# Performance work log

Hardware: AMD Instinct MI355X
Metric: run time of the kernel (lower is better)

## Reference

```python
import jax, jax.numpy as jnp
import numpy as np

N_WIRES = 12
DEPTH = 4
IN_DIM = 256
BATCH = 4096


def _apply_rx(state, theta, wire, n):
    """Apply RX(theta) = [[cos(t/2), -i sin(t/2)], [-i sin(t/2), cos(t/2)]] on `wire`.
    state: (batch, 2^n) complex. theta: scalar or (batch,) float."""
    half = theta * 0.5
    c = jnp.reshape(jnp.cos(half), (-1, 1, 1))  # broadcasts for scalar or per-batch
    s = jnp.reshape(jnp.sin(half), (-1, 1, 1))
    L, R = 2 ** wire, 2 ** (n - wire - 1)
    st = state.reshape(-1, L, 2, R)
    a0, a1 = st[:, :, 0], st[:, :, 1]
    b0 = c * a0 - 1j * s * a1
    b1 = -1j * s * a0 + c * a1
    return jnp.stack([b0, b1], axis=2).reshape(state.shape)


def _apply_cnot_adj(state, ctrl, n):
    """CNOT with control=ctrl, target=ctrl+1 (adjacent wires)."""
    L, R = 2 ** ctrl, 2 ** (n - ctrl - 2)
    st = state.reshape(-1, L, 2, 2, R)
    c0 = st[:, :, 0]
    c1 = st[:, :, 1, ::-1]  # flip target bit when control=1
    return jnp.stack([c0, c1], axis=2).reshape(state.shape)


def _pauli_z_signs(n):
    idx = np.arange(2 ** n)
    # wire 0 is the most-significant bit (torchquantum convention)
    bits = (idx[:, None] >> (n - 1 - np.arange(n))[None, :]) & 1
    return (1.0 - 2.0 * bits).astype(np.float32)  # (2^n, n)


def setup_inputs() -> dict:
    key = jax.random.key(0)
    k1, k2, k3 = jax.random.split(key, 3)
    x = jax.random.normal(k1, (BATCH, IN_DIM), dtype=jnp.float32)
    W = jax.random.normal(k2, (N_WIRES, IN_DIM), dtype=jnp.float32)
    params = jax.random.normal(k3, (DEPTH, N_WIRES, 1), dtype=jnp.float32)
    return {"x": x, "W": W, "params": params}


def reference(x, W, params):
    n = W.shape[0]
    depth = params.shape[0]
    batch = x.shape[0]
    angles = x @ W.T  # (batch, n) -- nn.Linear without bias
    state = jnp.zeros((batch, 2 ** n), dtype=jnp.complex64).at[:, 0].set(1.0)
    # data-encoding RX layer (per-batch angles)
    for w in range(n):
        state = _apply_rx(state, angles[:, w], w, n)
    # variational layers: RX(params) then CNOT ladder
    for d in range(depth):
        for w in range(n):
            state = _apply_rx(state, params[d, w, 0], w, n)
        for w in range(n - 1):
            state = _apply_cnot_adj(state, w, n)
    probs = jnp.real(state * jnp.conj(state))  # (batch, 2^n)
    signs = jnp.asarray(_pauli_z_signs(n))     # (2^n, n)
    return probs @ signs  # <Z_w> per wire, (batch, n)
```

## Files before the change

### kernel.cpp

```cpp
#include <hip/hip_runtime.h>
#include <math.h>

#define N_WIRES 12
#define DEPTH   4
#define IN_DIM  256
#define NK      4096
#define ROWS_PER_BLOCK 16
#define XSTRIDE 272


struct MaskTable {
    unsigned m[DEPTH * N_WIRES];
    unsigned S[N_WIRES];
};

__global__ __launch_bounds__(256)
void consts_kernel(const float* __restrict__ params, float* __restrict__ ws,
                   MaskTable mt)
{
    const int w = blockIdx.x;
    const int t = threadIdx.x;
    __shared__ float    thA[DEPTH * N_WIRES];
    __shared__ unsigned mAs[DEPTH * N_WIRES];
    __shared__ int      naS;
    __shared__ float    red[4][16];

    if (t == 0) {
        int na = 0;
        unsigned S = mt.S[w];
        for (int g = 0; g < DEPTH * N_WIRES; ++g)
            if (__popc(mt.m[g] & S) & 1) { mAs[na] = mt.m[g]; thA[na] = params[g]; ++na; }
        naS = na;
    }
    __syncthreads();
    const int na = naS;
    const unsigned S = mt.S[w];
    int pos[3], nb = 0;
    for (int b = 0; b < N_WIRES; ++b) if ((S >> b) & 1) pos[nb++] = b;

    float acc[16];
    #pragma unroll
    for (int c = 0; c < 16; ++c) acc[c] = 0.f;

    for (int i = 0; i < 16; ++i) {
        int k = (i << 8) | t;
        float P = 0.f;
        for (int g = 0; g < na; ++g) {
            float sgn = 1.f - 2.f * (float)(__popc(mAs[g] & (unsigned)k) & 1);
            P = fmaf(sgn, thA[g], P);
        }
        float sn, cs;
        sincosf(P, &sn, &cs);
        int kap = 0;
        for (int j = 0; j < nb; ++j) kap |= ((k >> pos[j]) & 1) << j;
        #pragma unroll
        for (int c = 0; c < 8; ++c) {
            acc[c]     += (c == kap) ? cs : 0.f;
            acc[c + 8] += (c == kap) ? sn : 0.f;
        }
    }
    #pragma unroll
    for (int c = 0; c < 16; ++c) {
        float v = acc[c];
        #pragma unroll
        for (int o = 1; o < 64; o <<= 1) v += __shfl_xor(v, o, 64);
        acc[c] = v;
    }
    const int lane = t & 63, wv = t >> 6;
    if (lane == 0)
        #pragma unroll
        for (int c = 0; c < 16; ++c) red[wv][c] = acc[c];
    __syncthreads();
    if (t < 16)
        ws[w * 16 + t] = red[0][t] + red[1][t] + red[2][t] + red[3][t];
}

__global__ __launch_bounds__(256)
void batch_kernel(const float* __restrict__ x, const float* __restrict__ W,
                  const float* __restrict__ ws, float* __restrict__ out,
                  MaskTable mt)
{
    __shared__ float xl[ROWS_PER_BLOCK * XSTRIDE];
    __shared__ float wl[N_WIRES * IN_DIM];
    __shared__ float al[ROWS_PER_BLOCK * N_WIRES];
    __shared__ float cl[N_WIRES * 16];
    const int t = threadIdx.x;
    const int rowbase = blockIdx.x * ROWS_PER_BLOCK;

    const float4* x4 = (const float4*)(x + (size_t)rowbase * IN_DIM);
    #pragma unroll
    for (int j = 0; j < 4; ++j) {
        int f   = t + 256 * j;
        int row = f >> 6;
        int c4  = f & 63;
        float4 v = x4[f];
        *(float4*)&xl[row * XSTRIDE + c4 * 4] = v;
    }
    const float4* W4 = (const float4*)W;
    #pragma unroll
    for (int j = 0; j < 3; ++j) {
        int f = t + 256 * j;
        ((float4*)wl)[f] = W4[f];
    }
    if (t < N_WIRES * 16) cl[t] = ws[t];
    __syncthreads();

    const int r = t >> 4, p = t & 15;
    float partial[N_WIRES];
    #pragma unroll
    for (int w = 0; w < N_WIRES; ++w) partial[w] = 0.f;
    for (int i = 0; i < 16; ++i) {
        float xv = xl[r * XSTRIDE + i * 16 + p];
        #pragma unroll
        for (int w = 0; w < N_WIRES; ++w)
            partial[w] = fmaf(xv, wl[w * IN_DIM + i * 16 + p], partial[w]);
    }
    #pragma unroll
    for (int w = 0; w < N_WIRES; ++w) {
        float v = partial[w];
        v += __shfl_xor(v, 1, 16);
        v += __shfl_xor(v, 2, 16);
        v += __shfl_xor(v, 4, 16);
        v += __shfl_xor(v, 8, 16);
        partial[w] = v;
    }
    if (p < N_WIRES) al[r * N_WIRES + p] = partial[p];
    __syncthreads();

    if (t < ROWS_PER_BLOCK * N_WIRES) {
        const int r2 = t / N_WIRES;
        const int w  = t - r2 * N_WIRES;
        unsigned S = mt.S[w];
        int pos[3], nb = 0;
        for (int b = 0; b < N_WIRES; ++b) if ((S >> b) & 1) pos[nb++] = b;
        float a[3] = {0.f, 0.f, 0.f};
        for (int j = 0; j < nb; ++j) a[j] = al[r2 * N_WIRES + pos[j]];
        float o = 0.f;
        const int nk = 1 << nb;
        for (int kap = 0; kap < nk; ++kap) {
            float B = 0.f;
            for (int j = 0; j < nb; ++j)
                B += ((kap >> j) & 1) ? -a[j] : a[j];
            float sn, cs;
            sincosf(B, &sn, &cs);
            o = fmaf(cs,  cl[w * 16 + kap],     o);
            o = fmaf(-sn, cl[w * 16 + 8 + kap], o);
        }
        out[(size_t)(rowbase + r2) * N_WIRES + w] = o * (1.f / 4096.f);
    }
}

static void gf2_mul(const unsigned* A, const unsigned* B, unsigned* C) {
    for (int i = 0; i < N_WIRES; ++i) {
        unsigned r = 0;
        for (int v = 0; v < N_WIRES; ++v)
            if ((A[i] >> v) & 1) r ^= B[v];
        C[i] = r;
    }
}

extern "C" void kernel_launch(void* const* d_in, const int* in_sizes, int n_in,
                              void* d_out, int out_size, void* d_ws, size_t ws_size,
                              hipStream_t stream) {
    const float* x      = (const float*)d_in[0];
    const float* W      = (const float*)d_in[1];
    const float* params = (const float*)d_in[2];
    float* out          = (float*)d_out;
    float* wsf          = (float*)d_ws;

    unsigned L[N_WIRES], Linv[N_WIRES];
    for (int w = 0; w < N_WIRES; ++w) {
        L[w]    = (1u << (w + 1)) - 1u;
        Linv[w] = (w == 0) ? 1u : ((1u << w) | (1u << (w - 1)));
    }
    unsigned Mp[DEPTH + 1][N_WIRES], Mi[DEPTH + 1][N_WIRES];
    for (int w = 0; w < N_WIRES; ++w) { Mp[0][w] = 1u << w; Mi[0][w] = 1u << w; }
    for (int d = 1; d <= DEPTH; ++d) {
        gf2_mul(L, Mp[d - 1], Mp[d]);
        gf2_mul(Linv, Mi[d - 1], Mi[d]);
    }

    MaskTable mt;
    for (int d = 0; d < DEPTH; ++d)
        for (int w = 0; w < N_WIRES; ++w) {
            unsigned m = 0;
            for (int u = 0; u < N_WIRES; ++u)
                if ((Mi[d][u] >> w) & 1) m |= (1u << u);
            mt.m[d * N_WIRES + w] = m;
        }
    for (int w = 0; w < N_WIRES; ++w) mt.S[w] = Mp[DEPTH][w];

    const int batch = in_sizes[0] / IN_DIM;

    hipLaunchKernelGGL(consts_kernel, dim3(N_WIRES), dim3(256), 0, stream,
                       params, wsf, mt);
    hipLaunchKernelGGL(batch_kernel, dim3(batch / ROWS_PER_BLOCK), dim3(256), 0, stream,
                       x, W, wsf, out, mt);
}
```

Baseline: 82.07 us.

## Parallelize constant computation across basis states with shared-memory atomic binning

The constants kernel now runs 16 blocks, each owning 256 basis indices. Each thread computes the phase for all 12 wires at once, using host-built 0/1 wire-gate weight tables, and bins cos/sin into shared memory with atomics. Before, it ran 12 blocks, one per wire, and looped serially over 4096 indices. The batch kernel sums the 16 per-block partials and switches to the fast __sincosf intrinsic, which trades some accuracy for speed.

```diff
diff --git a/kernel.cpp b/kernel.cpp
--- a/kernel.cpp
+++ b/kernel.cpp
@@ -3,82 +3,69 @@
 
 #define N_WIRES 12
 #define DEPTH   4
+#define NGATES  (DEPTH * N_WIRES)
 #define IN_DIM  256
-#define NK      4096
 #define ROWS_PER_BLOCK 16
 #define XSTRIDE 272
-
-
-struct MaskTable {
-    unsigned m[DEPTH * N_WIRES];
+#define K_BLOCKS 16
+
+
+struct ConstTab {
+    unsigned m[NGATES];
+    float    wt[N_WIRES][NGATES];
+    unsigned sh[N_WIRES][3];
+};
+struct MeasTab {
     unsigned S[N_WIRES];
 };
 
 __global__ __launch_bounds__(256)
 void consts_kernel(const float* __restrict__ params, float* __restrict__ ws,
-                   MaskTable mt)
+                   ConstTab ct)
 {
-    const int w = blockIdx.x;
+    __shared__ float acc[N_WIRES * 16];
     const int t = threadIdx.x;
-    __shared__ float    thA[DEPTH * N_WIRES];
-    __shared__ unsigned mAs[DEPTH * N_WIRES];
-    __shared__ int      naS;
-    __shared__ float    red[4][16];
-
-    if (t == 0) {
-        int na = 0;
-        unsigned S = mt.S[w];
-        for (int g = 0; g < DEPTH * N_WIRES; ++g)
-            if (__popc(mt.m[g] & S) & 1) { mAs[na] = mt.m[g]; thA[na] = params[g]; ++na; }
-        naS = na;
-    }
-    __syncthreads();
-    const int na = naS;
-    const unsigned S = mt.S[w];
-    int pos[3], nb = 0;
-    for (int b = 0; b < N_WIRES; ++b) if ((S >> b) & 1) pos[nb++] = b;
-
-    float acc[16];
-    #pragma unroll
-    for (int c = 0; c < 16; ++c) acc[c] = 0.f;
-
-    for (int i = 0; i < 16; ++i) {
-        int k = (i << 8) | t;
-        float P = 0.f;
-        for (int g = 0; g < na; ++g) {
-            float sgn = 1.f - 2.f * (float)(__popc(mAs[g] & (unsigned)k) & 1);
-            P = fmaf(sgn, thA[g], P);
-        }
+    if (t < N_WIRES * 16) acc[t] = 0.f;
+    __syncthreads();
+
+    const unsigned k = blockIdx.x * 256u + (unsigned)t;
+
+    float th[NGATES];
+    #pragma unroll
+    for (int g = 0; g < NGATES; ++g) th[g] = params[g];
+
+    float P[N_WIRES];
+    #pragma unroll
+    for (int w = 0; w < N_WIRES; ++w) P[w] = 0.f;
+
+    #pragma unroll
+    for (int g = 0; g < NGATES; ++g) {
+        unsigned par = (unsigned)(__popc(ct.m[g] & k) & 1);
+        float sg = __int_as_float(__float_as_int(th[g]) ^ (int)(par << 31));
+        #pragma unroll
+        for (int w = 0; w < N_WIRES; ++w)
+            P[w] = fmaf(sg, ct.wt[w][g], P[w]);
+    }
+
+    #pragma unroll
+    for (int w = 0; w < N_WIRES; ++w) {
         float sn, cs;
-        sincosf(P, &sn, &cs);
-        int kap = 0;
-        for (int j = 0; j < nb; ++j) kap |= ((k >> pos[j]) & 1) << j;
-        #pragma unroll
-        for (int c = 0; c < 8; ++c) {
-            acc[c]     += (c == kap) ? cs : 0.f;
-            acc[c + 8] += (c == kap) ? sn : 0.f;
-        }
-    }
-    #pragma unroll
-    for (int c = 0; c < 16; ++c) {
-        float v = acc[c];
-        #pragma unroll
-        for (int o = 1; o < 64; o <<= 1) v += __shfl_xor(v, o, 64);
-        acc[c] = v;
-    }
-    const int lane = t & 63, wv = t >> 6;
-    if (lane == 0)
-        #pragma unroll
-        for (int c = 0; c < 16; ++c) red[wv][c] = acc[c];
-    __syncthreads();
-    if (t < 16)
-        ws[w * 16 + t] = red[0][t] + red[1][t] + red[2][t] + red[3][t];
+        sincosf(P[w], &sn, &cs);
+        unsigned kap =  ((k >> ct.sh[w][0]) & 1u)
+                     | (((k >> ct.sh[w][1]) & 1u) << 1)
+                     | (((k >> ct.sh[w][2]) & 1u) << 2);
+        atomicAdd(&acc[w * 16 + kap], cs);
+        atomicAdd(&acc[w * 16 + 8 + kap], sn);
+    }
+    __syncthreads();
+    if (t < N_WIRES * 16)
+        ws[blockIdx.x * (N_WIRES * 16) + t] = acc[t];
 }
 
 __global__ __launch_bounds__(256)
 void batch_kernel(const float* __restrict__ x, const float* __restrict__ W,
                   const float* __restrict__ ws, float* __restrict__ out,
-                  MaskTable mt)
+                  MeasTab mt)
 {
     __shared__ float xl[ROWS_PER_BLOCK * XSTRIDE];
     __shared__ float wl[N_WIRES * IN_DIM];
@@ -102,7 +89,12 @@
         int f = t + 256 * j;
         ((float4*)wl)[f] = W4[f];
     }
-    if (t < N_WIRES * 16) cl[t] = ws[t];
+    if (t < N_WIRES * 16) {
+        float v = 0.f;
+        #pragma unroll
+        for (int p = 0; p < K_BLOCKS; ++p) v += ws[p * (N_WIRES * 16) + t];
+        cl[t] = v;
+    }
     __syncthreads();
 
     const int r = t >> 4, p = t & 15;
@@ -142,7 +134,7 @@
             for (int j = 0; j < nb; ++j)
                 B += ((kap >> j) & 1) ? -a[j] : a[j];
             float sn, cs;
-            sincosf(B, &sn, &cs);
+            __sincosf(B, &sn, &cs);
             o = fmaf(cs,  cl[w * 16 + kap],     o);
             o = fmaf(-sn, cl[w * 16 + 8 + kap], o);
         }
@@ -158,6 +150,7 @@
         C[i] = r;
     }
 }
+static int popc_host(unsigned v) { int c = 0; while (v) { c += v & 1; v >>= 1; } return c; }
 
 extern "C" void kernel_launch(void* const* d_in, const int* in_sizes, int n_in,
                               void* d_out, int out_size, void* d_ws, size_t ws_size,
@@ -180,20 +173,30 @@
         gf2_mul(Linv, Mi[d - 1], Mi[d]);
     }
 
-    MaskTable mt;
+    ConstTab ct;
+    MeasTab  mt;
     for (int d = 0; d < DEPTH; ++d)
         for (int w = 0; w < N_WIRES; ++w) {
             unsigned m = 0;
             for (int u = 0; u < N_WIRES; ++u)
                 if ((Mi[d][u] >> w) & 1) m |= (1u << u);
-            mt.m[d * N_WIRES + w] = m;
+            ct.m[d * N_WIRES + w] = m;
         }
     for (int w = 0; w < N_WIRES; ++w) mt.S[w] = Mp[DEPTH][w];
 
+    for (int w = 0; w < N_WIRES; ++w) {
+        for (int g = 0; g < NGATES; ++g)
+            ct.wt[w][g] = (popc_host(ct.m[g] & mt.S[w]) & 1) ? 1.f : 0.f;
+        int nb = 0;
+        for (int b = 0; b < N_WIRES; ++b)
+            if ((mt.S[w] >> b) & 1) ct.sh[w][nb++] = (unsigned)b;
+        for (; nb < 3; ++nb) ct.sh[w][nb] = 31u;
+    }
+
     const int batch = in_sizes[0] / IN_DIM;
 
-    hipLaunchKernelGGL(consts_kernel, dim3(N_WIRES), dim3(256), 0, stream,
-                       params, wsf, mt);
+    hipLaunchKernelGGL(consts_kernel, dim3(K_BLOCKS), dim3(256), 0, stream,
+                       params, wsf, ct);
     hipLaunchKernelGGL(batch_kernel, dim3(batch / ROWS_PER_BLOCK), dim3(256), 0, stream,
                        x, W, wsf, out, mt);
 }
```

New measurement: 75.39 us. 8.1% less time.
